# Kernel optimization log

Hardware: AMD Instinct MI355X
Metric: run time of the kernel (lower is better)

## Reference

```python
import jax, jax.numpy as jnp
import numpy as np

FEAT = 1433
HID = 2
NUM_CLASS = 7
EPS = 1e-5  # torch BatchNorm1d default eps


def _bn_softsign(h, gamma, beta):
    # BatchNorm1d in training mode: batch stats over (batch, length) per channel.
    mu = h.mean(axis=(0, 2), keepdims=True)
    var = h.var(axis=(0, 2), keepdims=True)  # biased, matches torch normalization
    hn = (h - mu) * jax.lax.rsqrt(var + EPS)
    hn = hn * gamma[None, :, None] + beta[None, :, None]
    return hn / (1.0 + jnp.abs(hn))  # Softsign


def feature_adjacency(x, y):
    # (x.unsqueeze(-1) * y.unsqueeze(-2)).sum(dim=1) with x channel dim == 1
    # reduces to an outer product of x[:,0] with neighbor.sum over K.
    adj = jnp.einsum('bf,bg->bfg', x.sum(1), y.sum(1))  # [B,F,F]
    adj = adj + jnp.swapaxes(adj, -1, -2)
    adj = jnp.sqrt(adj)
    # row_normalize: divide by sum over dim 1, zero out inf/nan
    norm = adj / adj.sum(axis=1, keepdims=True)
    norm = jnp.where(jnp.isfinite(norm), norm, 0.0)
    return norm + jnp.eye(FEAT, dtype=x.dtype)


def featbrd(x, adj, W, b):
    # adjacency-based feature conv: y[b,c,f] = sum_g adj[(b),f,g] x[b,c,g],
    # then 1x1 conv over channels (Conv1d kernel_size=1).
    if adj.shape[0] == 1:
        y = jnp.einsum('fg,bcg->bcf', adj[0], x)
    else:
        y = jnp.einsum('bfg,bcg->bcf', adj, x)
    return jnp.einsum('oc,bcf->bof', W, y) + b[None, :, None]


def setup_inputs() -> dict:
    key = jax.random.key(0)
    ks = jax.random.split(key, 10)
    B, K = 64, 8
    inp = {
        'x': jax.random.uniform(ks[0], (B, 1, FEAT), dtype=jnp.float32),
        'neighbor': jax.random.uniform(ks[1], (B, K, FEAT), dtype=jnp.float32),
        'adj_buf': jnp.zeros((1, FEAT, FEAT), jnp.float32),
        'W1': jax.random.normal(ks[2], (HID, 1), jnp.float32) * 0.5,
        'b1': jnp.zeros((HID,), jnp.float32),
        'W2': jax.random.normal(ks[3], (HID, HID), jnp.float32) * 0.5,
        'b2': jnp.zeros((HID,), jnp.float32),
        'g1': jnp.ones((HID,), jnp.float32),
        'be1': jnp.zeros((HID,), jnp.float32),
        'g2': jnp.ones((HID,), jnp.float32),
        'be2': jnp.zeros((HID,), jnp.float32),
        'Wc': jax.random.normal(ks[4], (NUM_CLASS, FEAT * HID), jnp.float32) * 0.02,
        'bc': jnp.zeros((NUM_CLASS,), jnp.float32),
    }
    return inp


def reference(x, neighbor, adj_buf, W1, b1, W2, b2, g1, be1, g2, be2, Wc, bc):
    fadj = feature_adjacency(x, neighbor)          # [B,F,F]
    adj_tot = adj_buf + fadj.sum(0)                # [1,F,F] (buffer starts at zero)
    h = _bn_softsign(featbrd(x, fadj, W1, b1), g1, be1)      # [B,HID,F]
    h = _bn_softsign(featbrd(h, adj_tot, W2, b2), g2, be2)   # [B,HID,F]
    flat = h.reshape(h.shape[0], -1)               # Flatten (C then F, row-major)
    return flat @ Wc.T + bc
```

## Files before the change

kernel.cpp:

```cpp
#include <hip/hip_runtime.h>
#include <hip/hip_bf16.h>
#include <math.h>

constexpr int F   = 1433;
constexpr int NB  = 64;
constexpr int KN  = 8;
constexpr int BF  = NB * F;
constexpr float EPS = 1e-5f;

constexpr int SF  = 16;
constexpr int CH  = 90;
constexpr int AbS = 1440;
constexpr int SK  = 15;
constexpr int FT  = 12;
constexpr int NA  = 720;
constexpr int NST = 256;

constexpr int O_YS  = 0;
constexpr int O_DP  = O_YS + BF;
constexpr int O_Y1P = O_DP + SF * BF;
constexpr int O_P   = O_Y1P + SF * BF;
constexpr int O_Y1  = O_P + 4 * BF;
constexpr int O_Y2  = O_Y1 + BF;
constexpr int O_G2P = O_Y2 + 2 * BF;
constexpr int O_AB  = O_G2P + SK * 128 * F;
constexpr int O_ST  = O_AB + (F * AbS) / 2;

__global__ __launch_bounds__(256) void k_ys(const float* __restrict__ nbr,
                                            float* __restrict__ ys,
                                            float* __restrict__ st) {
  if (blockIdx.x == 0 && threadIdx.x < 64) st[threadIdx.x] = 0.f;
  int i = blockIdx.x * 256 + threadIdx.x;
  if (i >= BF) return;
  int b = i / F, g = i - b * F;
  const float* p = nbr + (size_t)b * KN * F + g;
  float s = 0.f;
#pragma unroll
  for (int k = 0; k < KN; ++k) s += p[k * F];
  ys[i] = s;
}

__global__ __launch_bounds__(256) void k_D(const float* __restrict__ x,
                                           const float* __restrict__ ys,
                                           float* __restrict__ DP) {
  __shared__ __align__(8) float2 xyc[CH];
  const int b = blockIdx.x, s = blockIdx.y;
  const int cs = s * CH, cn = min(CH, F - cs);
  for (int i = threadIdx.x; i < cn; i += 256)
    xyc[i] = make_float2(x[b * F + cs + i], ys[b * F + cs + i]);
  __syncthreads();
  float gx[6], gy[6], acc[6] = {};
#pragma unroll
  for (int j = 0; j < 6; ++j) {
    int g = threadIdx.x + 256 * j;
    gx[j] = (g < F) ? x[b * F + g] : 0.f;
    gy[j] = (g < F) ? ys[b * F + g] : 0.f;
  }
#pragma unroll 6
  for (int i = 0; i < cn; ++i) {
    float2 p = xyc[i];
#pragma unroll
    for (int j = 0; j < 6; ++j)
      acc[j] += __builtin_amdgcn_sqrtf(fmaf(gy[j], p.x, gx[j] * p.y));
  }
#pragma unroll
  for (int j = 0; j < 6; ++j) {
    int g = threadIdx.x + 256 * j;
    if (g < F) DP[(size_t)s * BF + b * F + g] = acc[j];
  }
}

__global__ __launch_bounds__(256) void k_y1(const float* __restrict__ x,
                                            const float* __restrict__ ys,
                                            const float* __restrict__ DP,
                                            float* __restrict__ Y1P,
                                            float4* __restrict__ P) {
  __shared__ __align__(16) float4 pl[CH];
  const int b = blockIdx.x, s = blockIdx.y;
  const int cs = s * CH, cn = min(CH, F - cs);
  for (int i = threadIdx.x; i < cn; i += 256) {
    int g = cs + i;
    float d = 0.f;
#pragma unroll
    for (int t = 0; t < SF; ++t) d += DP[(size_t)t * BF + b * F + g];
    float inv = (d > 0.f) ? 1.f / d : 0.f;
    float xv = x[b * F + g], yv = ys[b * F + g];
    float4 pv = make_float4(xv, yv, xv * inv, inv);
    pl[i] = pv;
    P[b * F + g] = pv;
  }
  __syncthreads();
  float fx[6], fy[6], acc[6] = {};
#pragma unroll
  for (int j = 0; j < 6; ++j) {
    int f = threadIdx.x + 256 * j;
    fx[j] = (f < F) ? x[b * F + f] : 0.f;
    fy[j] = (f < F) ? ys[b * F + f] : 0.f;
  }
#pragma unroll 6
  for (int i = 0; i < cn; ++i) {
    float4 p = pl[i];
#pragma unroll
    for (int j = 0; j < 6; ++j)
      acc[j] = fmaf(__builtin_amdgcn_sqrtf(fmaf(fx[j], p.y, fy[j] * p.x)), p.z, acc[j]);
  }
#pragma unroll
  for (int j = 0; j < 6; ++j) {
    int f = threadIdx.x + 256 * j;
    if (f < F) Y1P[(size_t)s * BF + b * F + f] = acc[j];
  }
}

__global__ __launch_bounds__(256) void k_Astats(const float* __restrict__ x,
                                                const float* __restrict__ ys,
                                                const float4* __restrict__ P,
                                                const float* __restrict__ Y1P,
                                                __hip_bfloat16* __restrict__ Ab,
                                                float* __restrict__ y1,
                                                float* __restrict__ st) {
  const int bid = blockIdx.x;
  if (bid < NA) {
    __shared__ float2 fxy[FT][NB];
    const int gxc = bid % 6, fy = bid / 6;
    const int fbase = fy * FT;
#pragma unroll
    for (int r = 0; r < 3; ++r) {
      int i = threadIdx.x + 256 * r;
      int j = i >> 6, bb = i & 63;
      int f = fbase + j;
      float vx = 0.f, vy = 0.f;
      if (f < F) { vx = x[bb * F + f]; vy = ys[bb * F + f]; }
      fxy[j][bb] = make_float2(vx, vy);
    }
    __syncthreads();
    const int g = gxc * 256 + threadIdx.x;
    if (g >= AbS) return;
    if (g < F) {
      float acc[FT] = {};
      float4 pc = P[g];
#pragma unroll 2
      for (int bb = 0; bb < NB; ++bb) {
        float4 pn = pc;
        if (bb < NB - 1) pn = P[(bb + 1) * F + g];
#pragma unroll
        for (int j = 0; j < FT; ++j) {
          float2 w = fxy[j][bb];
          acc[j] = fmaf(__builtin_amdgcn_sqrtf(fmaf(w.x, pc.y, pc.x * w.y)), pc.w, acc[j]);
        }
        pc = pn;
      }
#pragma unroll
      for (int j = 0; j < FT; ++j) {
        int f = fbase + j;
        if (f < F) Ab[(size_t)f * AbS + g] = __float2bfloat16(acc[j]);
      }
    } else {
#pragma unroll
      for (int j = 0; j < FT; ++j) {
        int f = fbase + j;
        if (f < F) Ab[(size_t)f * AbS + g] = __float2bfloat16(0.f);
      }
    }
  } else {
    const int sid = bid - NA;
    float sv = 0.f, sq = 0.f;
    for (int i = sid * 256 + threadIdx.x; i < BF; i += NST * 256) {
      float v = x[i];
#pragma unroll
      for (int t = 0; t < SF; ++t) v += Y1P[(size_t)t * BF + i];
      y1[i] = v;
      sv += v; sq += v * v;
    }
#pragma unroll
    for (int o = 32; o; o >>= 1) {
      sv += __shfl_down(sv, o, 64);
      sq += __shfl_down(sq, o, 64);
    }
    __shared__ float ls[4], lq[4];
    int wave = threadIdx.x >> 6, lane = threadIdx.x & 63;
    if (lane == 0) { ls[wave] = sv; lq[wave] = sq; }
    __syncthreads();
    if (threadIdx.x == 0) {
      atomicAdd(&st[0], ls[0] + ls[1] + ls[2] + ls[3]);
      atomicAdd(&st[1], lq[0] + lq[1] + lq[2] + lq[3]);
    }
  }
}

__global__ __launch_bounds__(256) void k_gemm(const ushort* __restrict__ Ab,
                                              const float* __restrict__ y1,
                                              const float* __restrict__ st,
                                              const float* __restrict__ W1,
                                              const float* __restrict__ g1,
                                              const float* __restrict__ be1,
                                              float* __restrict__ G2P) {
  const float mu = st[0] / (float)BF;
  const float var = st[1] / (float)BF - mu * mu;
  const float wa = W1[0], wb = W1[1];
  const float k0 = wa * g1[0] / sqrtf(wa * wa * var + EPS);
  const float k1 = wb * g1[1] / sqrtf(wb * wb * var + EPS);
  const float c0 = -k0 * mu + be1[0];
  const float c1 = -k1 * mu + be1[1];

  __shared__ __align__(16) float Al[2][32 * 36];
  __shared__ __align__(16) float Hl[2][32 * 132];
  const int f0 = blockIdx.x * 32;
  const int gs = blockIdx.y * 96;
  const int tid = threadIdx.x;
  const int ffs = tid >> 3, g4s = (tid & 7) * 4;
  const int hb = tid & 7, hg = tid >> 3;
  const int fsub = (tid & 7) * 4, msub = (tid >> 3) * 4;

  uint2 pa; float pyv[8];
  auto loadRegs = [&](int gb) {
    const int f = f0 + ffs;
    pa = make_uint2(0u, 0u);
    if (f < F) pa = *(const uint2*)&Ab[(size_t)f * AbS + gb + g4s];
    const int gl = min(gb + hg, F - 1);
#pragma unroll
    for (int r = 0; r < 8; ++r) pyv[r] = y1[(hb + 8 * r) * F + gl];
  };
  auto storeLDS = [&](int buf) {
    Al[buf][(g4s + 0) * 36 + ffs] = __uint_as_float(pa.x << 16);
    Al[buf][(g4s + 1) * 36 + ffs] = __uint_as_float(pa.x & 0xffff0000u);
    Al[buf][(g4s + 2) * 36 + ffs] = __uint_as_float(pa.y << 16);
    Al[buf][(g4s + 3) * 36 + ffs] = __uint_as_float(pa.y & 0xffff0000u);
#pragma unroll
    for (int r = 0; r < 8; ++r) {
      const int bb = hb + 8 * r;
      const float v = pyv[r];
      float h0 = fmaf(k0, v, c0); h0 = h0 / (1.f + fabsf(h0));
      float h1 = fmaf(k1, v, c1); h1 = h1 / (1.f + fabsf(h1));
      *(float2*)&Hl[buf][hg * 132 + 2 * bb] = make_float2(h0, h1);
    }
  };

  float acc[4][4] = {};
  loadRegs(gs);
  storeLDS(0);
  __syncthreads();
  for (int c = 0; c < 3; ++c) {
    const int buf = c & 1;
    if (c < 2) loadRegs(gs + (c + 1) * 32);
    const float* A_ = Al[buf];
    const float* H_ = Hl[buf];
#pragma unroll 4
    for (int gi = 0; gi < 32; ++gi) {
      float4 a4 = *(const float4*)&A_[gi * 36 + fsub];
      float4 h4 = *(const float4*)&H_[gi * 132 + msub];
      float av[4] = {a4.x, a4.y, a4.z, a4.w};
      float hv[4] = {h4.x, h4.y, h4.z, h4.w};
#pragma unroll
      for (int i = 0; i < 4; ++i)
#pragma unroll
        for (int j = 0; j < 4; ++j)
          acc[i][j] = fmaf(av[i], hv[j], acc[i][j]);
    }
    if (c < 2) storeLDS(buf ^ 1);
    __syncthreads();
  }
  float* dst = G2P + (size_t)blockIdx.y * 128 * F;
#pragma unroll
  for (int i = 0; i < 4; ++i) {
    int f = f0 + fsub + i;
    if (f < F) {
#pragma unroll
      for (int j = 0; j < 4; ++j)
        dst[(msub + j) * F + f] = acc[i][j];
    }
  }
}

__global__ __launch_bounds__(256) void k_stats2(const float* __restrict__ y1,
                                                const float* __restrict__ G2P,
                                                const float* __restrict__ st,
                                                const float* __restrict__ W1,
                                                const float* __restrict__ g1,
                                                const float* __restrict__ be1,
                                                float* __restrict__ y2,
                                                float* __restrict__ stw) {
  const float mu = st[0] / (float)BF;
  const float var = st[1] / (float)BF - mu * mu;
  const float wa = W1[0], wb = W1[1];
  const float k0 = wa * g1[0] / sqrtf(wa * wa * var + EPS);
  const float k1 = wb * g1[1] / sqrtf(wb * wb * var + EPS);
  const float c0 = -k0 * mu + be1[0];
  const float c1 = -k1 * mu + be1[1];

  float su = 0.f, sv = 0.f, suu = 0.f, svv = 0.f, suv = 0.f;
  for (int i = blockIdx.x * 256 + threadIdx.x; i < BF; i += gridDim.x * 256) {
    int b = i / F, f = i - b * F;
    float w = y1[i];
    float h0 = fmaf(k0, w, c0); h0 = h0 / (1.f + fabsf(h0));
    float h1 = fmaf(k1, w, c1); h1 = h1 / (1.f + fabsf(h1));
    int iu = (2 * b) * F + f, iv = iu + F;
    float u = 64.f * h0, v = 64.f * h1;
#pragma unroll
    for (int t = 0; t < SK; ++t) {
      u += G2P[(size_t)t * 128 * F + iu];
      v += G2P[(size_t)t * 128 * F + iv];
    }
    y2[iu] = u; y2[iv] = v;
    su += u; sv += v; suu += u * u; svv += v * v; suv += u * v;
  }
#pragma unroll
  for (int o = 32; o; o >>= 1) {
    su += __shfl_down(su, o, 64);
    sv += __shfl_down(sv, o, 64);
    suu += __shfl_down(suu, o, 64);
    svv += __shfl_down(svv, o, 64);
    suv += __shfl_down(suv, o, 64);
  }
  __shared__ float red[5][4];
  int wave = threadIdx.x >> 6, lane = threadIdx.x & 63;
  if (lane == 0) {
    red[0][wave] = su; red[1][wave] = sv; red[2][wave] = suu;
    red[3][wave] = svv; red[4][wave] = suv;
  }
  __syncthreads();
  if (threadIdx.x == 0) {
#pragma unroll
    for (int m = 0; m < 5; ++m)
      atomicAdd(&stw[2 + m], red[m][0] + red[m][1] + red[m][2] + red[m][3]);
  }
}

__global__ __launch_bounds__(256) void k_out(const float* __restrict__ y2,
                                             const float* __restrict__ st,
                                             const float* __restrict__ W2,
                                             const float* __restrict__ b2,
                                             const float* __restrict__ g2,
                                             const float* __restrict__ be2,
                                             const float* __restrict__ Wc,
                                             const float* __restrict__ bc,
                                             float* __restrict__ out) {
  float n = (float)BF;
  float Eu = st[2] / n, Ev = st[3] / n;
  float Euu = st[4] / n, Evv = st[5] / n, Euv = st[6] / n;
  float cA[2], cB[2], cC[2];
#pragma unroll
  for (int o = 0; o < 2; ++o) {
    float w0 = W2[o * 2 + 0], w1 = W2[o * 2 + 1];
    float mean = w0 * Eu + w1 * Ev + b2[o];
    float Eh2 = w0 * w0 * Euu + 2.f * w0 * w1 * Euv + w1 * w1 * Evv +
                2.f * b2[o] * (w0 * Eu + w1 * Ev) + b2[o] * b2[o];
    float vr = Eh2 - mean * mean;
    float inv = g2[o] / sqrtf(vr + EPS);
    cA[o] = w0 * inv;
    cB[o] = w1 * inv;
    cC[o] = (b2[o] - mean) * inv + be2[o];
  }
  const int b = blockIdx.x;
  float acc[7] = {};
  for (int f = threadIdx.x; f < F; f += 256) {
    float u = y2[(2 * b) * F + f], v = y2[(2 * b + 1) * F + f];
    float h0 = fmaf(cA[0], u, fmaf(cB[0], v, cC[0]));
    h0 = h0 / (1.f + fabsf(h0));
    float h1 = fmaf(cA[1], u, fmaf(cB[1], v, cC[1]));
    h1 = h1 / (1.f + fabsf(h1));
#pragma unroll
    for (int o = 0; o < 7; ++o) acc[o] = fmaf(Wc[o * (2 * F) + f], h0, acc[o]);
#pragma unroll
    for (int o = 0; o < 7; ++o) acc[o] = fmaf(Wc[o * (2 * F) + F + f], h1, acc[o]);
  }
#pragma unroll
  for (int o = 0; o < 7; ++o) {
#pragma unroll
    for (int s = 32; s; s >>= 1) acc[o] += __shfl_down(acc[o], s, 64);
  }
  __shared__ float red[7][4];
  int wave = threadIdx.x >> 6, lane = threadIdx.x & 63;
  if (lane == 0) {
#pragma unroll
    for (int o = 0; o < 7; ++o) red[o][wave] = acc[o];
  }
  __syncthreads();
  if (threadIdx.x < 7) {
    int o = threadIdx.x;
    out[b * 7 + o] = red[o][0] + red[o][1] + red[o][2] + red[o][3] + bc[o];
  }
}

extern "C" void kernel_launch(void* const* d_in, const int* in_sizes, int n_in,
                              void* d_out, int out_size, void* d_ws, size_t ws_size,
                              hipStream_t stream) {
  const float* x    = (const float*)d_in[0];
  const float* nbr  = (const float*)d_in[1];
  const float* W1   = (const float*)d_in[3];
  const float* W2   = (const float*)d_in[5];
  const float* b2   = (const float*)d_in[6];
  const float* g1   = (const float*)d_in[7];
  const float* be1  = (const float*)d_in[8];
  const float* g2   = (const float*)d_in[9];
  const float* be2  = (const float*)d_in[10];
  const float* Wc   = (const float*)d_in[11];
  const float* bc   = (const float*)d_in[12];
  float* out = (float*)d_out;
  float* ws  = (float*)d_ws;

  float*  ys  = ws + O_YS;
  float*  DP  = ws + O_DP;
  float*  Y1P = ws + O_Y1P;
  float4* P   = (float4*)(ws + O_P);
  float*  y1  = ws + O_Y1;
  float*  y2  = ws + O_Y2;
  float*  G2P = ws + O_G2P;
  __hip_bfloat16* Ab = (__hip_bfloat16*)(ws + O_AB);
  float*  st  = ws + O_ST;

  k_ys    <<<(BF + 255) / 256, 256, 0, stream>>>(nbr, ys, st);
  k_D     <<<dim3(NB, SF), 256, 0, stream>>>(x, ys, DP);
  k_y1    <<<dim3(NB, SF), 256, 0, stream>>>(x, ys, DP, Y1P, P);
  k_Astats<<<NA + NST, 256, 0, stream>>>(x, ys, P, Y1P, Ab, y1, st);
  k_gemm  <<<dim3(45, SK), 256, 0, stream>>>((const ushort*)Ab, y1, st, W1, g1, be1, G2P);
  k_stats2<<<NST, 256, 0, stream>>>(y1, G2P, st, W1, g1, be1, y2, st);
  k_out   <<<NB, 256, 0, stream>>>(y2, st, W2, b2, g2, be2, Wc, bc, out);
}
```

Before: 208.2 us.

## Replace split-K partial buffer with atomic accumulation into y2 and deepen P prefetch

The GEMM's split-K partials now go straight into y2 through float atomicAdd instead of being written to a 15-slice G2P buffer that k_stats2 then summed. y2 is zeroed inside k_y1, and k_stats2 reads the accumulated value once. This removes the large partial-buffer write and read traffic, at the cost of atomic contention and a summation order that is no longer deterministic. Separately, the adjacency-build loop in k_Astats now prefetches P four batch rows at a time instead of one, to hide more load latency.

```diff
diff --git a/kernel.cpp b/kernel.cpp
--- a/kernel.cpp
+++ b/kernel.cpp
@@ -22,8 +22,7 @@
 constexpr int O_P   = O_Y1P + SF * BF;
 constexpr int O_Y1  = O_P + 4 * BF;
 constexpr int O_Y2  = O_Y1 + BF;
-constexpr int O_G2P = O_Y2 + 2 * BF;
-constexpr int O_AB  = O_G2P + SK * 128 * F;
+constexpr int O_AB  = O_Y2 + 2 * BF;
 constexpr int O_ST  = O_AB + (F * AbS) / 2;
 
 __global__ __launch_bounds__(256) void k_ys(const float* __restrict__ nbr,
@@ -74,7 +73,12 @@
                                             const float* __restrict__ ys,
                                             const float* __restrict__ DP,
                                             float* __restrict__ Y1P,
-                                            float4* __restrict__ P) {
+                                            float4* __restrict__ P,
+                                            float* __restrict__ y2) {
+  {
+    int zid = (blockIdx.y * NB + blockIdx.x) * 256 + threadIdx.x;
+    if (zid < 2 * BF) y2[zid] = 0.f;
+  }
   __shared__ __align__(16) float4 pl[CH];
   const int b = blockIdx.x, s = blockIdx.y;
   const int cs = s * CH, cn = min(CH, F - cs);
@@ -137,17 +141,25 @@
     if (g >= AbS) return;
     if (g < F) {
       float acc[FT] = {};
-      float4 pc = P[g];
-#pragma unroll 2
-      for (int bb = 0; bb < NB; ++bb) {
-        float4 pn = pc;
-        if (bb < NB - 1) pn = P[(bb + 1) * F + g];
-#pragma unroll
-        for (int j = 0; j < FT; ++j) {
-          float2 w = fxy[j][bb];
-          acc[j] = fmaf(__builtin_amdgcn_sqrtf(fmaf(w.x, pc.y, pc.x * w.y)), pc.w, acc[j]);
+      float4 cur[4], nxt[4];
+#pragma unroll
+      for (int t = 0; t < 4; ++t) cur[t] = P[t * F + g];
+      for (int bb = 0; bb < NB; bb += 4) {
+        if (bb + 4 < NB) {
+#pragma unroll
+          for (int t = 0; t < 4; ++t) nxt[t] = P[(bb + 4 + t) * F + g];
         }
-        pc = pn;
+#pragma unroll
+        for (int t = 0; t < 4; ++t) {
+          float4 pc = cur[t];
+#pragma unroll
+          for (int j = 0; j < FT; ++j) {
+            float2 w = fxy[j][bb + t];
+            acc[j] = fmaf(__builtin_amdgcn_sqrtf(fmaf(w.x, pc.y, pc.x * w.y)), pc.w, acc[j]);
+          }
+        }
+#pragma unroll
+        for (int t = 0; t < 4; ++t) cur[t] = nxt[t];
       }
 #pragma unroll
       for (int j = 0; j < FT; ++j) {
@@ -193,7 +205,7 @@
                                               const float* __restrict__ W1,
                                               const float* __restrict__ g1,
                                               const float* __restrict__ be1,
-                                              float* __restrict__ G2P) {
+                                              float* __restrict__ y2) {
   const float mu = st[0] / (float)BF;
   const float var = st[1] / (float)BF - mu * mu;
   const float wa = W1[0], wb = W1[1];
@@ -259,20 +271,18 @@
     if (c < 2) storeLDS(buf ^ 1);
     __syncthreads();
   }
-  float* dst = G2P + (size_t)blockIdx.y * 128 * F;
 #pragma unroll
   for (int i = 0; i < 4; ++i) {
     int f = f0 + fsub + i;
     if (f < F) {
 #pragma unroll
       for (int j = 0; j < 4; ++j)
-        dst[(msub + j) * F + f] = acc[i][j];
+        atomicAdd(&y2[(msub + j) * F + f], acc[i][j]);
     }
   }
 }
 
 __global__ __launch_bounds__(256) void k_stats2(const float* __restrict__ y1,
-                                                const float* __restrict__ G2P,
                                                 const float* __restrict__ st,
                                                 const float* __restrict__ W1,
                                                 const float* __restrict__ g1,
@@ -294,12 +304,8 @@
     float h0 = fmaf(k0, w, c0); h0 = h0 / (1.f + fabsf(h0));
     float h1 = fmaf(k1, w, c1); h1 = h1 / (1.f + fabsf(h1));
     int iu = (2 * b) * F + f, iv = iu + F;
-    float u = 64.f * h0, v = 64.f * h1;
-#pragma unroll
-    for (int t = 0; t < SK; ++t) {
-      u += G2P[(size_t)t * 128 * F + iu];
-      v += G2P[(size_t)t * 128 * F + iv];
-    }
+    float u = y2[iu] + 64.f * h0;
+    float v = y2[iv] + 64.f * h1;
     y2[iu] = u; y2[iv] = v;
     su += u; sv += v; suu += u * u; svv += v * v; suv += u * v;
   }
@@ -404,15 +410,14 @@
   float4* P   = (float4*)(ws + O_P);
   float*  y1  = ws + O_Y1;
   float*  y2  = ws + O_Y2;
-  float*  G2P = ws + O_G2P;
   __hip_bfloat16* Ab = (__hip_bfloat16*)(ws + O_AB);
   float*  st  = ws + O_ST;
 
   k_ys    <<<(BF + 255) / 256, 256, 0, stream>>>(nbr, ys, st);
   k_D     <<<dim3(NB, SF), 256, 0, stream>>>(x, ys, DP);
-  k_y1    <<<dim3(NB, SF), 256, 0, stream>>>(x, ys, DP, Y1P, P);
+  k_y1    <<<dim3(NB, SF), 256, 0, stream>>>(x, ys, DP, Y1P, P, y2);
   k_Astats<<<NA + NST, 256, 0, stream>>>(x, ys, P, Y1P, Ab, y1, st);
-  k_gemm  <<<dim3(45, SK), 256, 0, stream>>>((const ushort*)Ab, y1, st, W1, g1, be1, G2P);
-  k_stats2<<<NST, 256, 0, stream>>>(y1, G2P, st, W1, g1, be1, y2, st);
+  k_gemm  <<<dim3(45, SK), 256, 0, stream>>>((const ushort*)Ab, y1, st, W1, g1, be1, y2);
+  k_stats2<<<NST, 256, 0, stream>>>(y1, st, W1, g1, be1, y2, st);
   k_out   <<<NB, 256, 0, stream>>>(y2, st, W2, b2, g2, be2, Wc, bc, out);
 }
```

After: 241.1 us. +15.8%, slower.

## Fuse summed-adjacency tile generation into the second-layer GEMM, drop bf16 buffer

Applied to the files above, without the earlier changes.

The separate kernel that built the batch-summed adjacency matrix in bf16 and wrote it to global memory is removed. Each GEMM block now recomputes its 32x32 adjacency tile on the fly from the per-batch P vectors (sqrt of x/ys cross terms weighted by p.w) before multiplying with the softsign activations. This removes the global write and read of the F×F bf16 buffer and one launch, and restores fp32 precision for the adjacency. In exchange every tile is recomputed once per grid column, with 64 batch terms per element, and the LDS double buffering is dropped. The four f-side P loads per batch step also come straight from global memory.

```diff
diff --git a/kernel.cpp b/kernel.cpp
--- a/kernel.cpp
+++ b/kernel.cpp
@@ -10,10 +10,7 @@
 
 constexpr int SF  = 16;
 constexpr int CH  = 90;
-constexpr int AbS = 1440;
 constexpr int SK  = 15;
-constexpr int FT  = 12;
-constexpr int NA  = 720;
 constexpr int NST = 256;
 
 constexpr int O_YS  = 0;
@@ -23,8 +20,7 @@
 constexpr int O_Y1  = O_P + 4 * BF;
 constexpr int O_Y2  = O_Y1 + BF;
 constexpr int O_G2P = O_Y2 + 2 * BF;
-constexpr int O_AB  = O_G2P + SK * 128 * F;
-constexpr int O_ST  = O_AB + (F * AbS) / 2;
+constexpr int O_ST  = O_G2P + SK * 128 * F;
 
 __global__ __launch_bounds__(256) void k_ys(const float* __restrict__ nbr,
                                             float* __restrict__ ys,
@@ -111,89 +107,40 @@
   }
 }
 
-__global__ __launch_bounds__(256) void k_Astats(const float* __restrict__ x,
-                                                const float* __restrict__ ys,
-                                                const float4* __restrict__ P,
-                                                const float* __restrict__ Y1P,
-                                                __hip_bfloat16* __restrict__ Ab,
-                                                float* __restrict__ y1,
-                                                float* __restrict__ st) {
-  const int bid = blockIdx.x;
-  if (bid < NA) {
-    __shared__ float2 fxy[FT][NB];
-    const int gxc = bid % 6, fy = bid / 6;
-    const int fbase = fy * FT;
-#pragma unroll
-    for (int r = 0; r < 3; ++r) {
-      int i = threadIdx.x + 256 * r;
-      int j = i >> 6, bb = i & 63;
-      int f = fbase + j;
-      float vx = 0.f, vy = 0.f;
-      if (f < F) { vx = x[bb * F + f]; vy = ys[bb * F + f]; }
-      fxy[j][bb] = make_float2(vx, vy);
-    }
-    __syncthreads();
-    const int g = gxc * 256 + threadIdx.x;
-    if (g >= AbS) return;
-    if (g < F) {
-      float acc[FT] = {};
-      float4 pc = P[g];
-#pragma unroll 2
-      for (int bb = 0; bb < NB; ++bb) {
-        float4 pn = pc;
-        if (bb < NB - 1) pn = P[(bb + 1) * F + g];
-#pragma unroll
-        for (int j = 0; j < FT; ++j) {
-          float2 w = fxy[j][bb];
-          acc[j] = fmaf(__builtin_amdgcn_sqrtf(fmaf(w.x, pc.y, pc.x * w.y)), pc.w, acc[j]);
-        }
-        pc = pn;
-      }
-#pragma unroll
-      for (int j = 0; j < FT; ++j) {
-        int f = fbase + j;
-        if (f < F) Ab[(size_t)f * AbS + g] = __float2bfloat16(acc[j]);
-      }
-    } else {
-#pragma unroll
-      for (int j = 0; j < FT; ++j) {
-        int f = fbase + j;
-        if (f < F) Ab[(size_t)f * AbS + g] = __float2bfloat16(0.f);
-      }
-    }
-  } else {
-    const int sid = bid - NA;
-    float sv = 0.f, sq = 0.f;
-    for (int i = sid * 256 + threadIdx.x; i < BF; i += NST * 256) {
-      float v = x[i];
-#pragma unroll
-      for (int t = 0; t < SF; ++t) v += Y1P[(size_t)t * BF + i];
-      y1[i] = v;
-      sv += v; sq += v * v;
-    }
-#pragma unroll
-    for (int o = 32; o; o >>= 1) {
-      sv += __shfl_down(sv, o, 64);
-      sq += __shfl_down(sq, o, 64);
-    }
-    __shared__ float ls[4], lq[4];
-    int wave = threadIdx.x >> 6, lane = threadIdx.x & 63;
-    if (lane == 0) { ls[wave] = sv; lq[wave] = sq; }
-    __syncthreads();
-    if (threadIdx.x == 0) {
-      atomicAdd(&st[0], ls[0] + ls[1] + ls[2] + ls[3]);
-      atomicAdd(&st[1], lq[0] + lq[1] + lq[2] + lq[3]);
-    }
-  }
-}
-
-__global__ __launch_bounds__(256) void k_gemm(const ushort* __restrict__ Ab,
-                                              const float* __restrict__ y1,
-                                              const float* __restrict__ st,
-                                              const float* __restrict__ W1,
-                                              const float* __restrict__ g1,
-                                              const float* __restrict__ be1,
-                                              float* __restrict__ G2P) {
+__global__ __launch_bounds__(256) void k_s1(const float* __restrict__ x,
+                                            const float* __restrict__ Y1P,
+                                            float* __restrict__ y1,
+                                            float* __restrict__ st) {
+  float sv = 0.f, sq = 0.f;
+  for (int i = blockIdx.x * 256 + threadIdx.x; i < BF; i += NST * 256) {
+    float v = x[i];
+#pragma unroll
+    for (int t = 0; t < SF; ++t) v += Y1P[(size_t)t * BF + i];
+    y1[i] = v;
+    sv += v; sq += v * v;
+  }
+#pragma unroll
+  for (int o = 32; o; o >>= 1) {
+    sv += __shfl_down(sv, o, 64);
+    sq += __shfl_down(sq, o, 64);
+  }
+  __shared__ float ls[4], lq[4];
+  int wave = threadIdx.x >> 6, lane = threadIdx.x & 63;
+  if (lane == 0) { ls[wave] = sv; lq[wave] = sq; }
+  __syncthreads();
+  if (threadIdx.x == 0) {
+    atomicAdd(&st[0], ls[0] + ls[1] + ls[2] + ls[3]);
+    atomicAdd(&st[1], lq[0] + lq[1] + lq[2] + lq[3]);
+  }
+}
+
+__global__ __launch_bounds__(256, 4) void k_gemmA(const float4* __restrict__ P,
+                                                  const float* __restrict__ y1,
+                                                  const float* __restrict__ st,
+                                                  const float* __restrict__ W1,
+                                                  const float* __restrict__ g1,
+                                                  const float* __restrict__ be1,
+                                                  float* __restrict__ G2P) {
   const float mu = st[0] / (float)BF;
   const float var = st[1] / (float)BF - mu * mu;
   const float wa = W1[0], wb = W1[1];
@@ -202,52 +149,77 @@
   const float c0 = -k0 * mu + be1[0];
   const float c1 = -k1 * mu + be1[1];
 
-  __shared__ __align__(16) float Al[2][32 * 36];
-  __shared__ __align__(16) float Hl[2][32 * 132];
+  __shared__ __align__(16) float4 Pb[32 * 32];
+  __shared__ __align__(16) float Al[32 * 36];
+  __shared__ __align__(16) float Hl[32 * 132];
   const int f0 = blockIdx.x * 32;
   const int gs = blockIdx.y * 96;
   const int tid = threadIdx.x;
-  const int ffs = tid >> 3, g4s = (tid & 7) * 4;
+  const int git = tid >> 3;
+  const int fq  = tid & 7;
+  const int fsub = fq * 4;
+  const int msub = (tid >> 3) * 4;
   const int hb = tid & 7, hg = tid >> 3;
-  const int fsub = (tid & 7) * 4, msub = (tid >> 3) * 4;
-
-  uint2 pa; float pyv[8];
-  auto loadRegs = [&](int gb) {
-    const int f = f0 + ffs;
-    pa = make_uint2(0u, 0u);
-    if (f < F) pa = *(const uint2*)&Ab[(size_t)f * AbS + gb + g4s];
-    const int gl = min(gb + hg, F - 1);
-#pragma unroll
-    for (int r = 0; r < 8; ++r) pyv[r] = y1[(hb + 8 * r) * F + gl];
-  };
-  auto storeLDS = [&](int buf) {
-    Al[buf][(g4s + 0) * 36 + ffs] = __uint_as_float(pa.x << 16);
-    Al[buf][(g4s + 1) * 36 + ffs] = __uint_as_float(pa.x & 0xffff0000u);
-    Al[buf][(g4s + 2) * 36 + ffs] = __uint_as_float(pa.y << 16);
-    Al[buf][(g4s + 3) * 36 + ffs] = __uint_as_float(pa.y & 0xffff0000u);
-#pragma unroll
-    for (int r = 0; r < 8; ++r) {
-      const int bb = hb + 8 * r;
-      const float v = pyv[r];
-      float h0 = fmaf(k0, v, c0); h0 = h0 / (1.f + fabsf(h0));
-      float h1 = fmaf(k1, v, c1); h1 = h1 / (1.f + fabsf(h1));
-      *(float2*)&Hl[buf][hg * 132 + 2 * bb] = make_float2(h0, h1);
-    }
-  };
+
+  float xf[4], yf[4];
+#pragma unroll
+  for (int j = 0; j < 4; ++j) {
+    int f = min(f0 + fsub + j, F - 1);
+    xf[j] = P[f].x;
+    yf[j] = P[f].y;
+  }
 
   float acc[4][4] = {};
-  loadRegs(gs);
-  storeLDS(0);
-  __syncthreads();
   for (int c = 0; c < 3; ++c) {
-    const int buf = c & 1;
-    if (c < 2) loadRegs(gs + (c + 1) * 32);
-    const float* A_ = Al[buf];
-    const float* H_ = Hl[buf];
+    const int gb = gs + c * 32;
+    float a[4] = {0.f, 0.f, 0.f, 0.f};
+    for (int half = 0; half < 2; ++half) {
+      const int b0 = half * 32;
+      __syncthreads();
+#pragma unroll
+      for (int r = 0; r < 4; ++r) {
+        int idx = tid + 256 * r;
+        int bb = idx >> 5, gg = idx & 31;
+        int g = gb + gg;
+        float4 pv = P[(size_t)(b0 + bb) * F + min(g, F - 1)];
+        if (g >= F) pv.w = 0.f;
+        Pb[bb * 32 + gg] = pv;
+      }
+      __syncthreads();
+      for (int bb = 0; bb < 32; ++bb) {
+        const int b = b0 + bb;
+        float4 pf0 = P[(size_t)b * F + min(f0 + fsub + 0, F - 1)];
+        float4 pf1 = P[(size_t)b * F + min(f0 + fsub + 1, F - 1)];
+        float4 pf2 = P[(size_t)b * F + min(f0 + fsub + 2, F - 1)];
+        float4 pf3 = P[(size_t)b * F + min(f0 + fsub + 3, F - 1)];
+        float4 pg = Pb[bb * 32 + git];
+        float t0 = fmaf(pf0.x, pg.y, pf0.y * pg.x);
+        float t1 = fmaf(pf1.x, pg.y, pf1.y * pg.x);
+        float t2 = fmaf(pf2.x, pg.y, pf2.y * pg.x);
+        float t3 = fmaf(pf3.x, pg.y, pf3.y * pg.x);
+        a[0] = fmaf(__builtin_amdgcn_sqrtf(t0), pg.w, a[0]);
+        a[1] = fmaf(__builtin_amdgcn_sqrtf(t1), pg.w, a[1]);
+        a[2] = fmaf(__builtin_amdgcn_sqrtf(t2), pg.w, a[2]);
+        a[3] = fmaf(__builtin_amdgcn_sqrtf(t3), pg.w, a[3]);
+      }
+    }
+    *(float4*)&Al[git * 36 + fsub] = make_float4(a[0], a[1], a[2], a[3]);
+    {
+      const int gl = min(gb + hg, F - 1);
+#pragma unroll
+      for (int r = 0; r < 8; ++r) {
+        const int bb = hb + 8 * r;
+        const float v = y1[bb * F + gl];
+        float h0 = fmaf(k0, v, c0); h0 = h0 / (1.f + fabsf(h0));
+        float h1 = fmaf(k1, v, c1); h1 = h1 / (1.f + fabsf(h1));
+        *(float2*)&Hl[hg * 132 + 2 * bb] = make_float2(h0, h1);
+      }
+    }
+    __syncthreads();
 #pragma unroll 4
     for (int gi = 0; gi < 32; ++gi) {
-      float4 a4 = *(const float4*)&A_[gi * 36 + fsub];
-      float4 h4 = *(const float4*)&H_[gi * 132 + msub];
+      float4 a4 = *(const float4*)&Al[gi * 36 + fsub];
+      float4 h4 = *(const float4*)&Hl[gi * 132 + msub];
       float av[4] = {a4.x, a4.y, a4.z, a4.w};
       float hv[4] = {h4.x, h4.y, h4.z, h4.w};
 #pragma unroll
@@ -256,8 +228,6 @@
         for (int j = 0; j < 4; ++j)
           acc[i][j] = fmaf(av[i], hv[j], acc[i][j]);
     }
-    if (c < 2) storeLDS(buf ^ 1);
-    __syncthreads();
   }
   float* dst = G2P + (size_t)blockIdx.y * 128 * F;
 #pragma unroll
@@ -405,14 +375,13 @@
   float*  y1  = ws + O_Y1;
   float*  y2  = ws + O_Y2;
   float*  G2P = ws + O_G2P;
-  __hip_bfloat16* Ab = (__hip_bfloat16*)(ws + O_AB);
   float*  st  = ws + O_ST;
 
   k_ys    <<<(BF + 255) / 256, 256, 0, stream>>>(nbr, ys, st);
   k_D     <<<dim3(NB, SF), 256, 0, stream>>>(x, ys, DP);
   k_y1    <<<dim3(NB, SF), 256, 0, stream>>>(x, ys, DP, Y1P, P);
-  k_Astats<<<NA + NST, 256, 0, stream>>>(x, ys, P, Y1P, Ab, y1, st);
-  k_gemm  <<<dim3(45, SK), 256, 0, stream>>>((const ushort*)Ab, y1, st, W1, g1, be1, G2P);
+  k_s1    <<<NST, 256, 0, stream>>>(x, Y1P, y1, st);
+  k_gemmA <<<dim3(45, SK), 256, 0, stream>>>(P, y1, st, W1, g1, be1, G2P);
   k_stats2<<<NST, 256, 0, stream>>>(y1, G2P, st, W1, g1, be1, y2, st);
   k_out   <<<NB, 256, 0, stream>>>(y2, st, W2, b2, g2, be2, Wc, bc, out);
 }
```

Result: slower. 308.8 us (+48.3%).
